# Performance work log

Measured on AMD Instinct MI355X. Metric: run time of the kernel, lower is better.

The kernel has to match this reference:

```python
import jax, jax.numpy as jnp
import numpy as np

N_CLUSTERS = 100
ALPHA = 1.0
NDF = 256
IN_DIM = 1024 * 8 * 8  # i3d_nch * os * os
BN, SN = 32, 64


def setup_inputs() -> dict:
    key = jax.random.key(0)
    k1, k2, k3, k4 = jax.random.split(key, 4)
    z_roi = jax.random.normal(k1, (BN, SN, IN_DIM), dtype=jnp.float32)
    mask = jnp.ones((BN, SN), dtype=bool)
    w_emb = jax.random.normal(k2, (IN_DIM, NDF), dtype=jnp.float32) * 0.02
    b_emb = jnp.zeros((NDF,), dtype=jnp.float32)
    centroids = jax.random.normal(k3, (N_CLUSTERS, NDF), dtype=jnp.float32)
    return {"z_roi": z_roi, "mask": mask, "w_emb": w_emb,
            "b_emb": b_emb, "centroids": centroids}


def _student_t(z, centroids):
    # z: [bn, sn, d]; centroids: [K, d]
    # pairwise L2 distance (NOT squared, matching torch.linalg.vector_norm)
    d2 = ((z * z).sum(-1, keepdims=True)
          + (centroids * centroids).sum(-1)
          - 2.0 * jnp.einsum("bsd,kd->bsk", z, centroids))  # [bn, sn, K]
    dist = jnp.sqrt(jnp.clip(d2, 0.0))
    s_tmp = (1.0 + dist / ALPHA) ** (-(ALPHA + 1.0) / 2.0)
    return s_tmp / s_tmp.sum(-1, keepdims=True)


def reference(z_roi, mask, w_emb, b_emb, centroids):
    # visual embedding: Linear(i3d_nch*os*os -> ndf)
    z = jnp.einsum("bsi,io->bso", z_roi, w_emb) + b_emb  # [bn, sn, ndf]
    m = mask[..., None]
    s = jnp.where(m, _student_t(z, centroids), 0.0)       # [bn, sn, K]
    z_all = jnp.where(m, z, 0.0)                           # detached copy in torch
    c = jnp.argmax(s, axis=2)                              # [bn, sn]
    return z_all, s, c
```

## Files before the change

kernel.cpp:

```cpp
#include <hip/hip_runtime.h>
#include <math.h>

#define MROWS 2048
#define NCOLS 256
#define KDIM  65536
#define NCLU  100

#define BM 128
#define BN 128
#define BK 32
#define SPLITK 16
#define KCHUNK (KDIM / SPLITK)
#define SA 132
#define SB 128

#define BMT 128
#define BNT 128
#define BKT 32
#define NSTEP (KCHUNK / BKT)
#define LDT 40
#define BTILE 16384

typedef _Float16 half8  __attribute__((ext_vector_type(8)));
typedef _Float16 half4v __attribute__((ext_vector_type(4)));
typedef float    f32x4  __attribute__((ext_vector_type(4)));

#define GLD_LDS16(g, l) __builtin_amdgcn_global_load_lds(                      \
    (__attribute__((address_space(1))) void*)(g),                              \
    (__attribute__((address_space(3))) void*)(l), 16, 0, 0)

__global__ __launch_bounds__(256, 4)
void prep_b_kernel(const float* __restrict__ B, unsigned char* __restrict__ Bws)
{
    __shared__ float Ts[BKT][132];
    const int t    = threadIdx.x;
    const int step = blockIdx.x;
    const int ks   = blockIdx.y;
    const int bnb  = blockIdx.z;

    const int kbase = ks * KCHUNK + step * BKT;
    const int nbase = bnb * 128;

    #pragma unroll
    for (int r = 0; r < 4; ++r) {
        const int fidx = r * 256 + t;
        const int k  = fidx >> 5;
        const int c4 = fidx & 31;
        const float4 v = *(const float4*)(B + (size_t)(kbase + k) * NCOLS + nbase + c4 * 4);
        *(float4*)&Ts[k][c4 * 4] = v;
    }
    __syncthreads();

    unsigned char* outT = Bws + (size_t)((bnb * SPLITK + ks) * NSTEP + step) * BTILE;
    #pragma unroll
    for (int r = 0; r < 4; ++r) {
        const int oidx = r * 256 + t;
        const int n  = oidx >> 3;
        const int X  = oidx & 7;
        const int LX = X ^ (n & 7);
        const int mtx = LX >> 2;
        const int kb  = (LX & 3) * 8;
        half8 hv;
        #pragma unroll
        for (int j = 0; j < 8; ++j) {
            const float v = Ts[kb + j][n];
            const _Float16 h = (_Float16)v;
            hv[j] = mtx ? (_Float16)(v - (float)h) : h;
        }
        *(half8*)(outT + n * 128 + X * 16) = hv;
    }
}

__global__ __launch_bounds__(256, 2)
void gemm_mfma_kernel(const float* __restrict__ A,
                      const unsigned char* __restrict__ Bws,
                      float* __restrict__ C)
{
    __shared__ _Float16 As[2][BMT][LDT];
    __shared__ __align__(16) unsigned char Bs[2][BTILE];

    const int t    = threadIdx.x;
    const int lane = t & 63;
    const int wid  = t >> 6;
    const int wm   = wid >> 1;
    const int wn   = wid & 1;

    const int bm  = blockIdx.x;
    const int bnb = blockIdx.y;
    const int ks  = blockIdx.z;

    const float* Ab = A + (size_t)bm * BMT * KDIM + (size_t)ks * KCHUNK;
    const unsigned char* Bb = Bws + (size_t)((bnb * SPLITK + ks) * NSTEP) * BTILE;

    const int am  = t >> 3;
    const int akf = (t & 7) * 4;

    const int r16  = lane & 15;
    const int kb16 = lane >> 4;

    int bhoff[4], bloff[4];
    #pragma unroll
    for (int nf = 0; nf < 4; ++nf) {
        const int n    = wn * 64 + nf * 16 + r16;
        const int mask = (n & 7) << 4;
        bhoff[nf] = n * 128 + ((kb16 * 16) ^ mask);
        bloff[nf] = n * 128 + ((64 + kb16 * 16) ^ mask);
    }

    f32x4 acc[4][4] = {};
    float4 pA[4];

    #pragma unroll
    for (int i = 0; i < 4; ++i)
        pA[i] = *(const float4*)(Ab + (size_t)(am + 32 * i) * KDIM + akf);
    #pragma unroll
    for (int r = 0; r < 4; ++r)
        GLD_LDS16(Bb + (size_t)(r * 256 + t) * 16,
                  &Bs[0][(r * 256 + wid * 64) * 16]);
    #pragma unroll
    for (int i = 0; i < 4; ++i) {
        half4v h;
        h[0] = (_Float16)pA[i].x; h[1] = (_Float16)pA[i].y;
        h[2] = (_Float16)pA[i].z; h[3] = (_Float16)pA[i].w;
        *(half4v*)&As[0][am + 32 * i][akf] = h;
    }
    __syncthreads();

    int cb = 0;
    for (int step = 0; step < NSTEP; ++step) {
        const int nb = cb ^ 1;
        const bool pf = (step + 1) < NSTEP;

        if (pf) {
            const int kk = (step + 1) * BKT;
            #pragma unroll
            for (int i = 0; i < 4; ++i)
                pA[i] = *(const float4*)(Ab + (size_t)(am + 32 * i) * KDIM + kk + akf);
            const unsigned char* Bt = Bb + (size_t)(step + 1) * BTILE;
            #pragma unroll
            for (int r = 0; r < 4; ++r)
                GLD_LDS16(Bt + (size_t)(r * 256 + t) * 16,
                          &Bs[nb][(r * 256 + wid * 64) * 16]);
        }

        half8 av[4], bh[4], bl[4];
        #pragma unroll
        for (int mf = 0; mf < 4; ++mf)
            av[mf] = *(const half8*)&As[cb][wm * 64 + mf * 16 + r16][kb16 * 8];
        #pragma unroll
        for (int nf = 0; nf < 4; ++nf) {
            bh[nf] = *(const half8*)&Bs[cb][bhoff[nf]];
            bl[nf] = *(const half8*)&Bs[cb][bloff[nf]];
        }
        #pragma unroll
        for (int mf = 0; mf < 4; ++mf)
            #pragma unroll
            for (int nf = 0; nf < 4; ++nf) {
                acc[mf][nf] = __builtin_amdgcn_mfma_f32_16x16x32_f16(av[mf], bh[nf], acc[mf][nf], 0, 0, 0);
                acc[mf][nf] = __builtin_amdgcn_mfma_f32_16x16x32_f16(av[mf], bl[nf], acc[mf][nf], 0, 0, 0);
            }

        if (pf) {
            #pragma unroll
            for (int i = 0; i < 4; ++i) {
                half4v h;
                h[0] = (_Float16)pA[i].x; h[1] = (_Float16)pA[i].y;
                h[2] = (_Float16)pA[i].z; h[3] = (_Float16)pA[i].w;
                *(half4v*)&As[nb][am + 32 * i][akf] = h;
            }
        }
        __syncthreads();
        cb = nb;
    }

    const int row0 = bm * BMT + wm * 64 + (lane >> 4) * 4;
    const int col0 = bnb * BNT + wn * 64 + r16;
    #pragma unroll
    for (int mf = 0; mf < 4; ++mf)
        #pragma unroll
        for (int nf = 0; nf < 4; ++nf)
            #pragma unroll
            for (int r = 0; r < 4; ++r)
                atomicAdd(&C[(size_t)(row0 + mf * 16 + r) * NCOLS + col0 + nf * 16],
                          acc[mf][nf][r]);
}

__global__ __launch_bounds__(256, 2)
void gemm_splitk_kernel(const float* __restrict__ A, const float* __restrict__ B,
                        float* __restrict__ C)
{
    __shared__ float As[BK][SA];
    __shared__ float Bs[BK][SB];

    const int t  = threadIdx.x;
    const int tx = t & 15;
    const int ty = t >> 4;

    const int bm = blockIdx.x;
    const int bn = blockIdx.y;
    const int bs = blockIdx.z;

    const float* Ab = A + (size_t)bm * BM * KDIM + (size_t)bs * KCHUNK;
    const float* Bb = B + (size_t)bs * KCHUNK * NCOLS + bn * BN;

    const int arow = t >> 3;
    const int akf4 = t & 7;
    const int bkr  = t >> 5;
    const int bnf4 = t & 31;

    float acc[8][8];
    #pragma unroll
    for (int i = 0; i < 8; ++i)
        #pragma unroll
        for (int j = 0; j < 8; ++j) acc[i][j] = 0.f;

    for (int kk = 0; kk < KCHUNK; kk += BK) {
        #pragma unroll
        for (int i = 0; i < 4; ++i) {
            const int r = arow + 32 * i;
            const float4 v = *(const float4*)(Ab + (size_t)r * KDIM + kk + akf4 * 4);
            As[akf4 * 4 + 0][r] = v.x;
            As[akf4 * 4 + 1][r] = v.y;
            As[akf4 * 4 + 2][r] = v.z;
            As[akf4 * 4 + 3][r] = v.w;
        }
        #pragma unroll
        for (int i = 0; i < 4; ++i) {
            const int r = bkr + 8 * i;
            *(float4*)&Bs[r][bnf4 * 4] =
                *(const float4*)(Bb + (size_t)(kk + r) * NCOLS + bnf4 * 4);
        }
        __syncthreads();

        #pragma unroll 8
        for (int k = 0; k < BK; ++k) {
            float a[8], b[8];
            *(float4*)&a[0] = *(const float4*)&As[k][ty * 4];
            *(float4*)&a[4] = *(const float4*)&As[k][64 + ty * 4];
            *(float4*)&b[0] = *(const float4*)&Bs[k][tx * 4];
            *(float4*)&b[4] = *(const float4*)&Bs[k][64 + tx * 4];
            #pragma unroll
            for (int i = 0; i < 8; ++i)
                #pragma unroll
                for (int j = 0; j < 8; ++j)
                    acc[i][j] = fmaf(a[i], b[j], acc[i][j]);
        }
        __syncthreads();
    }

    #pragma unroll
    for (int i = 0; i < 8; ++i) {
        const int row = bm * BM + ty * 4 + (i & 3) + 64 * (i >> 2);
        #pragma unroll
        for (int j = 0; j < 8; ++j) {
            const int col = bn * BN + tx * 4 + (j & 3) + 64 * (j >> 2);
            atomicAdd(&C[(size_t)row * NCOLS + col], acc[i][j]);
        }
    }
}

#define RPB 8

__global__ __launch_bounds__(256, 1)
void student_t_kernel(float* __restrict__ zbuf,
                      const int* __restrict__ mask,
                      const float* __restrict__ b_emb,
                      const float* __restrict__ cent,
                      float* __restrict__ s_out,
                      float* __restrict__ c_out)
{
    __shared__ float cs[50][257];
    __shared__ float zs[RPB][256];
    __shared__ float stbuf[RPB][128];
    __shared__ float c2[NCLU];
    __shared__ float z2s[RPB];
    __shared__ float redbuf[4];
    __shared__ float r_sum, r_idx;

    const int t    = threadIdx.x;
    const int wid  = t >> 6;
    const int lane = t & 63;
    const int row0 = blockIdx.x * RPB;

    const float bt = b_emb[t];

    if (t >= 100 && t < 128) {
        #pragma unroll
        for (int r = 0; r < RPB; ++r) stbuf[r][t] = 0.f;
    }

    for (int r = 0; r < RPB; ++r) {
        const int row = row0 + r;
        const float z = zbuf[(size_t)row * NCOLS + t] + bt;
        const bool m = mask[row] != 0;
        zbuf[(size_t)row * NCOLS + t] = m ? z : 0.f;
        zs[r][t] = z;
        float v = z * z;
        #pragma unroll
        for (int off = 32; off > 0; off >>= 1) v += __shfl_down(v, off, 64);
        if (lane == 0) redbuf[wid] = v;
        __syncthreads();
        if (t == 0) z2s[r] = redbuf[0] + redbuf[1] + redbuf[2] + redbuf[3];
        __syncthreads();
    }

    for (int ch = 0; ch < 2; ++ch) {
        const int kbase = ch * 50;
        for (int i = t; i < 50 * 256; i += 256) {
            const int k = i >> 8;
            const int d = i & 255;
            cs[k][d] = cent[(size_t)(kbase + k) * 256 + d];
        }
        __syncthreads();
        if (t < 50) {
            float s = 0.f;
            for (int d = 0; d < 256; ++d) s = fmaf(cs[t][d], cs[t][d], s);
            c2[kbase + t] = s;
        }
        __syncthreads();
        for (int rp = 0; rp < RPB / 2; ++rp) {
            if (t < 100) {
                const int r = rp * 2 + t / 50;
                const int k = t % 50;
                float dot = 0.f;
                for (int d = 0; d < 256; ++d)
                    dot = fmaf(zs[r][d], cs[k][d], dot);
                const float d2   = z2s[r] + c2[kbase + k] - 2.f * dot;
                const float dist = sqrtf(fmaxf(d2, 0.f));
                stbuf[r][kbase + k] = 1.f / (1.f + dist);
            }
        }
        __syncthreads();
    }

    for (int r = 0; r < RPB; ++r) {
        const int row = row0 + r;
        if (wid == 0) {
            const float v1 = stbuf[r][lane];
            const float v2 = stbuf[r][lane + 64];
            float sv = v1 + v2;
            #pragma unroll
            for (int off = 32; off > 0; off >>= 1) sv += __shfl_down(sv, off, 64);
            float mv; int mi;
            if (v2 > v1) { mv = v2; mi = lane + 64; } else { mv = v1; mi = lane; }
            #pragma unroll
            for (int off = 32; off > 0; off >>= 1) {
                const float ov = __shfl_down(mv, off, 64);
                const int   oi = __shfl_down(mi, off, 64);
                if (ov > mv || (ov == mv && oi < mi)) { mv = ov; mi = oi; }
            }
            if (lane == 0) { r_sum = sv; r_idx = (float)mi; }
        }
        __syncthreads();
        const bool m = mask[row] != 0;
        if (t < NCLU) s_out[(size_t)row * NCLU + t] = m ? stbuf[r][t] / r_sum : 0.f;
        if (t == 0)   c_out[row] = m ? r_idx : 0.f;
        __syncthreads();
    }
}

extern "C" void kernel_launch(void* const* d_in, const int* in_sizes, int n_in,
                              void* d_out, int out_size, void* d_ws, size_t ws_size,
                              hipStream_t stream)
{
    const float* z_roi = (const float*)d_in[0];
    const int*   mask  = (const int*)d_in[1];
    const float* w_emb = (const float*)d_in[2];
    const float* b_emb = (const float*)d_in[3];
    const float* cent  = (const float*)d_in[4];

    float* out   = (float*)d_out;
    float* z_all = out;
    float* s_out = out + (size_t)MROWS * NCOLS;
    float* c_out = s_out + (size_t)MROWS * NCLU;

    hipMemsetAsync(z_all, 0, (size_t)MROWS * NCOLS * sizeof(float), stream);

    const size_t ws_need = (size_t)2 * SPLITK * NSTEP * BTILE;

    if (ws_size >= ws_need) {
        unsigned char* bws = (unsigned char*)d_ws;
        prep_b_kernel<<<dim3(NSTEP, SPLITK, 2), 256, 0, stream>>>(w_emb, bws);
        gemm_mfma_kernel<<<dim3(MROWS / BMT, NCOLS / BNT, SPLITK), 256, 0, stream>>>(
            z_roi, bws, z_all);
    } else {
        gemm_splitk_kernel<<<dim3(MROWS / BM, NCOLS / BN, SPLITK), 256, 0, stream>>>(
            z_roi, w_emb, z_all);
    }

    student_t_kernel<<<dim3(MROWS / RPB), 256, 0, stream>>>(z_all, mask, b_emb, cent,
                                                            s_out, c_out);
}
```

Measured before the change: 1.019 ms.

## Load A fragments directly to registers and triple-buffer B with deeper prefetch

The GEMM no longer stages A through shared memory. Each lane loads its MFMA fragment of A straight from global memory and converts it to fp16 in registers. B moves to a three-deep LDS ring with prefetch two steps ahead, and manual vmcnt waits plus raw barriers replace __syncthreads. The aim is to remove the A LDS writes, reads and bank traffic and to hide more global latency, at the cost of more registers and uncoalesced per-lane A loads (32-byte chunks spread across rows).

```diff
diff --git a/kernel.cpp b/kernel.cpp
--- a/kernel.cpp
+++ b/kernel.cpp
@@ -18,11 +18,9 @@
 #define BNT 128
 #define BKT 32
 #define NSTEP (KCHUNK / BKT)
-#define LDT 40
 #define BTILE 16384
 
 typedef _Float16 half8  __attribute__((ext_vector_type(8)));
-typedef _Float16 half4v __attribute__((ext_vector_type(4)));
 typedef float    f32x4  __attribute__((ext_vector_type(4)));
 
 #define GLD_LDS16(g, l) __builtin_amdgcn_global_load_lds(                      \
@@ -76,8 +74,7 @@
                       const unsigned char* __restrict__ Bws,
                       float* __restrict__ C)
 {
-    __shared__ _Float16 As[2][BMT][LDT];
-    __shared__ __align__(16) unsigned char Bs[2][BTILE];
+    __shared__ __align__(16) unsigned char Bs[3][BTILE];
 
     const int t    = threadIdx.x;
     const int lane = t & 63;
@@ -92,11 +89,13 @@
     const float* Ab = A + (size_t)bm * BMT * KDIM + (size_t)ks * KCHUNK;
     const unsigned char* Bb = Bws + (size_t)((bnb * SPLITK + ks) * NSTEP) * BTILE;
 
-    const int am  = t >> 3;
-    const int akf = (t & 7) * 4;
-
     const int r16  = lane & 15;
     const int kb16 = lane >> 4;
+
+    const float* Arow[4];
+    #pragma unroll
+    for (int mf = 0; mf < 4; ++mf)
+        Arow[mf] = Ab + (size_t)(wm * 64 + mf * 16 + r16) * KDIM + kb16 * 8;
 
     int bhoff[4], bloff[4];
     #pragma unroll
@@ -108,69 +107,96 @@
     }
 
     f32x4 acc[4][4] = {};
-    float4 pA[4];
-
-    #pragma unroll
-    for (int i = 0; i < 4; ++i)
-        pA[i] = *(const float4*)(Ab + (size_t)(am + 32 * i) * KDIM + akf);
+    float4 pA0[8], pA1[8];
+    half8  av0[4], av1[4];
+
+    unsigned char* b0 = &Bs[0][0];
+    unsigned char* b1 = &Bs[1][0];
+    unsigned char* b2 = &Bs[2][0];
+
+    #pragma unroll
+    for (int mf = 0; mf < 4; ++mf) {
+        pA0[2 * mf]     = *(const float4*)(Arow[mf] + 0);
+        pA0[2 * mf + 1] = *(const float4*)(Arow[mf] + 4);
+    }
     #pragma unroll
     for (int r = 0; r < 4; ++r)
-        GLD_LDS16(Bb + (size_t)(r * 256 + t) * 16,
-                  &Bs[0][(r * 256 + wid * 64) * 16]);
-    #pragma unroll
-    for (int i = 0; i < 4; ++i) {
-        half4v h;
-        h[0] = (_Float16)pA[i].x; h[1] = (_Float16)pA[i].y;
-        h[2] = (_Float16)pA[i].z; h[3] = (_Float16)pA[i].w;
-        *(half4v*)&As[0][am + 32 * i][akf] = h;
-    }
-    __syncthreads();
-
-    int cb = 0;
-    for (int step = 0; step < NSTEP; ++step) {
-        const int nb = cb ^ 1;
-        const bool pf = (step + 1) < NSTEP;
-
-        if (pf) {
-            const int kk = (step + 1) * BKT;
-            #pragma unroll
-            for (int i = 0; i < 4; ++i)
-                pA[i] = *(const float4*)(Ab + (size_t)(am + 32 * i) * KDIM + kk + akf);
-            const unsigned char* Bt = Bb + (size_t)(step + 1) * BTILE;
+        GLD_LDS16(Bb + (size_t)(r * 256 + t) * 16, b0 + (r * 256 + wid * 64) * 16);
+    #pragma unroll
+    for (int mf = 0; mf < 4; ++mf) {
+        pA1[2 * mf]     = *(const float4*)(Arow[mf] + BKT + 0);
+        pA1[2 * mf + 1] = *(const float4*)(Arow[mf] + BKT + 4);
+    }
+    {
+        const unsigned char* Bt = Bb + (size_t)1 * BTILE;
+        #pragma unroll
+        for (int r = 0; r < 4; ++r)
+            GLD_LDS16(Bt + (size_t)(r * 256 + t) * 16, b1 + (r * 256 + wid * 64) * 16);
+    }
+    #pragma unroll
+    for (int mf = 0; mf < 4; ++mf) {
+        half8 h;
+        h[0] = (_Float16)pA0[2 * mf].x;     h[1] = (_Float16)pA0[2 * mf].y;
+        h[2] = (_Float16)pA0[2 * mf].z;     h[3] = (_Float16)pA0[2 * mf].w;
+        h[4] = (_Float16)pA0[2 * mf + 1].x; h[5] = (_Float16)pA0[2 * mf + 1].y;
+        h[6] = (_Float16)pA0[2 * mf + 1].z; h[7] = (_Float16)pA0[2 * mf + 1].w;
+        av0[mf] = h;
+    }
+    asm volatile("s_waitcnt vmcnt(12)" ::: "memory");
+    __builtin_amdgcn_s_barrier();
+    __builtin_amdgcn_sched_barrier(0);
+
+    auto STEP = [&](int S, float4 (&PF)[8], float4 (&PC)[8],
+                    half8 (&AC)[4], half8 (&AN)[4]) {
+        if (S + 2 < NSTEP) {
+            const int kk2 = (S + 2) * BKT;
+            #pragma unroll
+            for (int mf = 0; mf < 4; ++mf) {
+                PF[2 * mf]     = *(const float4*)(Arow[mf] + kk2 + 0);
+                PF[2 * mf + 1] = *(const float4*)(Arow[mf] + kk2 + 4);
+            }
+            const unsigned char* Bt = Bb + (size_t)(S + 2) * BTILE;
             #pragma unroll
             for (int r = 0; r < 4; ++r)
                 GLD_LDS16(Bt + (size_t)(r * 256 + t) * 16,
-                          &Bs[nb][(r * 256 + wid * 64) * 16]);
-        }
-
-        half8 av[4], bh[4], bl[4];
+                          b2 + (r * 256 + wid * 64) * 16);
+        }
+
+        half8 bh[4], bl[4];
+        #pragma unroll
+        for (int nf = 0; nf < 4; ++nf) {
+            bh[nf] = *(const half8*)(b0 + bhoff[nf]);
+            bl[nf] = *(const half8*)(b0 + bloff[nf]);
+        }
         #pragma unroll
         for (int mf = 0; mf < 4; ++mf)
-            av[mf] = *(const half8*)&As[cb][wm * 64 + mf * 16 + r16][kb16 * 8];
-        #pragma unroll
-        for (int nf = 0; nf < 4; ++nf) {
-            bh[nf] = *(const half8*)&Bs[cb][bhoff[nf]];
-            bl[nf] = *(const half8*)&Bs[cb][bloff[nf]];
-        }
-        #pragma unroll
-        for (int mf = 0; mf < 4; ++mf)
             #pragma unroll
             for (int nf = 0; nf < 4; ++nf) {
-                acc[mf][nf] = __builtin_amdgcn_mfma_f32_16x16x32_f16(av[mf], bh[nf], acc[mf][nf], 0, 0, 0);
-                acc[mf][nf] = __builtin_amdgcn_mfma_f32_16x16x32_f16(av[mf], bl[nf], acc[mf][nf], 0, 0, 0);
+                acc[mf][nf] = __builtin_amdgcn_mfma_f32_16x16x32_f16(AC[mf], bh[nf], acc[mf][nf], 0, 0, 0);
+                acc[mf][nf] = __builtin_amdgcn_mfma_f32_16x16x32_f16(AC[mf], bl[nf], acc[mf][nf], 0, 0, 0);
             }
 
-        if (pf) {
-            #pragma unroll
-            for (int i = 0; i < 4; ++i) {
-                half4v h;
-                h[0] = (_Float16)pA[i].x; h[1] = (_Float16)pA[i].y;
-                h[2] = (_Float16)pA[i].z; h[3] = (_Float16)pA[i].w;
-                *(half4v*)&As[nb][am + 32 * i][akf] = h;
+        if (S + 1 < NSTEP) {
+            #pragma unroll
+            for (int mf = 0; mf < 4; ++mf) {
+                half8 h;
+                h[0] = (_Float16)PC[2 * mf].x;     h[1] = (_Float16)PC[2 * mf].y;
+                h[2] = (_Float16)PC[2 * mf].z;     h[3] = (_Float16)PC[2 * mf].w;
+                h[4] = (_Float16)PC[2 * mf + 1].x; h[5] = (_Float16)PC[2 * mf + 1].y;
+                h[6] = (_Float16)PC[2 * mf + 1].z; h[7] = (_Float16)PC[2 * mf + 1].w;
+                AN[mf] = h;
             }
-        }
-        __syncthreads();
-        cb = nb;
+            if (S + 2 < NSTEP) asm volatile("s_waitcnt vmcnt(12)" ::: "memory");
+            else               asm volatile("s_waitcnt vmcnt(0)"  ::: "memory");
+        }
+        __builtin_amdgcn_s_barrier();
+        __builtin_amdgcn_sched_barrier(0);
+        unsigned char* tmp = b0; b0 = b1; b1 = b2; b2 = tmp;
+    };
+
+    for (int s = 0; s < NSTEP; s += 2) {
+        STEP(s,     pA0, pA1, av0, av1);
+        STEP(s + 1, pA1, pA0, av1, av0);
     }
 
     const int row0 = bm * BMT + wm * 64 + (lane >> 4) * 4;
```

New measurement: 960.2 us. 1.06x faster.
